# Performance work log

Measured on AMD Instinct MI355X. Metric: run time of the kernel, lower is better.

The kernel has to match this reference:

```python
import jax, jax.numpy as jnp
import numpy as np

N = 100000
E = 3200000
F_IN = 512
H = 128
C = 40


def gcn_conv(x, edge_index, edge_weight, W, b):
    """PyG GCNConv: x' = D^-1/2 (A+I) D^-1/2 (x W) + b, symmetric norm with self-loops."""
    n = x.shape[0]
    x = x @ W  # [N, H]
    row, col = edge_index[0], edge_index[1]
    sl = jnp.arange(n)
    row_f = jnp.concatenate([row, sl])
    col_f = jnp.concatenate([col, sl])
    w_f = jnp.concatenate([edge_weight, jnp.ones((n,), x.dtype)])
    deg = jax.ops.segment_sum(w_f, col_f, num_segments=n)  # in-degree incl. self-loop
    dinv = jnp.where(deg > 0, jax.lax.rsqrt(deg), 0.0)
    norm = dinv[row_f] * w_f * dinv[col_f]  # [E+N]
    msg = x[row_f] * norm[:, None]          # gather + scale
    out = jax.ops.segment_sum(msg, col_f, num_segments=n)  # scatter-add to targets
    return out + b


def setup_inputs() -> dict:
    key = jax.random.key(0)
    ks = jax.random.split(key, 12)
    inp = {
        "x": jax.random.normal(ks[0], (N, F_IN), jnp.float32),
        "edge_index": jax.random.randint(ks[1], (2, E), 0, N, jnp.int64),
        "edge_weight": jax.random.uniform(ks[2], (E,), jnp.float32),
        # first_lin
        "W1": jax.random.normal(ks[3], (F_IN, H), jnp.float32) / np.sqrt(F_IN),
        "b1": jnp.zeros((H,), jnp.float32),
        # conv layers (num_layers=2)
        "Wc1": jax.random.normal(ks[4], (H, H), jnp.float32) / np.sqrt(H),
        "bc1": jnp.zeros((H,), jnp.float32),
        "Wc2": jax.random.normal(ks[5], (H, H), jnp.float32) / np.sqrt(H),
        "bc2": jnp.zeros((H,), jnp.float32),
        # lin2
        "W2": jax.random.normal(ks[6], (H, C), jnp.float32) / np.sqrt(H),
        "b2": jnp.zeros((C,), jnp.float32),
        # wide layer
        "Ww": jax.random.normal(ks[7], (F_IN, C), jnp.float32) / np.sqrt(F_IN),
        "bw": jnp.zeros((C,), jnp.float32),
        # attention layer (-> 2 logits per node)
        "Wa": jax.random.normal(ks[8], (F_IN, 2), jnp.float32) / np.sqrt(F_IN),
        "ba": jnp.zeros((2,), jnp.float32),
    }
    return inp


def reference(x, edge_index, edge_weight, W1, b1, Wc1, bc1, Wc2, bc2, W2, b2, Ww, bw, Wa, ba):
    # deep branch (res_type=0.0, eval mode: dropout = identity)
    h = jax.nn.relu(x @ W1 + b1)
    h = jax.nn.relu(gcn_conv(h, edge_index, edge_weight, Wc1, bc1))
    h = jax.nn.relu(gcn_conv(h, edge_index, edge_weight, Wc2, bc2))
    deep_x = h @ W2 + b2  # [N, C]
    # wide branch on raw features
    wide_x = x @ Ww + bw  # [N, C]
    # attention fusion: softmax over 2 branch logits per node
    attn = jax.nn.softmax(x @ Wa + ba, axis=-1)  # [N, 2]
    out = deep_x * attn[:, 0:1] + wide_x * attn[:, 1:2]
    return out
```

## Files before the change

### kernel.cpp

```cpp
#include <hip/hip_runtime.h>
#include <hip/hip_bf16.h>
#include <cstdint>

#define N_NODES 100000
#define N_EDGES 3200000

typedef __attribute__((ext_vector_type(8))) short short8;
typedef __attribute__((ext_vector_type(4))) float floatx4;

#define FXS 8388608.0f
#define EA 320
#define EPB 10000
#define NBKT 391

__device__ __forceinline__ unsigned short f2bf(float f) {
    unsigned u = __float_as_uint(f);
    u += 0x7fff + ((u >> 16) & 1);
    return (unsigned short)(u >> 16);
}
__device__ __forceinline__ float bf2f(unsigned short s) {
    return __uint_as_float(((unsigned)s) << 16);
}
__device__ __forceinline__ float bflo(unsigned u) {
    return __uint_as_float(u << 16);
}
__device__ __forceinline__ float bfhi(unsigned u) {
    return __uint_as_float(u & 0xffff0000u);
}
__device__ __forceinline__ unsigned pack_bf2(float a, float b) {
    union { __hip_bfloat162 h2; unsigned u; } cv;
    cv.h2 = __float22bfloat162_rn(make_float2(a, b));
    return cv.u;
}

__global__ void setup_misc(const float* __restrict__ W1, const float* __restrict__ b1,
                           const float* __restrict__ Ww, const float* __restrict__ bw,
                           const float* __restrict__ Wa, const float* __restrict__ ba,
                           const float* __restrict__ Wc1, const float* __restrict__ Wc2,
                           const float* __restrict__ W2,
                           unsigned short* __restrict__ WcatT, float* __restrict__ bcat,
                           unsigned short* __restrict__ Wc1T, unsigned short* __restrict__ Wc2T,
                           unsigned short* __restrict__ W2T) {
    int bid = blockIdx.x, tid = threadIdx.x;
    if (bid < 192) {
        int c = bid;
        for (int kk = tid; kk < 512; kk += 256) {
            float v;
            if (c < 128)      v = W1[kk * 128 + c];
            else if (c < 168) v = Ww[kk * 40 + (c - 128)];
            else if (c < 170) v = Wa[kk * 2 + (c - 168)];
            else              v = 0.f;
            WcatT[(size_t)c * 512 + kk] = f2bf(v);
        }
        if (tid == 0) {
            float b;
            if (c < 128)      b = b1[c];
            else if (c < 168) b = bw[c - 128];
            else if (c < 170) b = ba[c - 168];
            else              b = 0.f;
            bcat[c] = b;
        }
    } else if (bid < 320) {
        int c = bid - 192;
        if (tid < 128) Wc1T[(size_t)c * 128 + tid] = f2bf(Wc1[tid * 128 + c]);
        else { int k = tid - 128; Wc2T[(size_t)c * 128 + k] = f2bf(Wc2[k * 128 + c]); }
    } else {
        int c = bid - 320;
        if (tid < 128)
            W2T[(size_t)c * 128 + tid] = (c < 40) ? f2bf(W2[tid * 40 + c])
                                                  : (unsigned short)0;
    }
}

template <int EPI, int NT, int AF32>
__device__ __forceinline__ void gemm_body(
    int mblk, const void* __restrict__ Avoid, const unsigned short* __restrict__ BT,
    int M, int K,
    unsigned short* __restrict__ C0, float* __restrict__ C1, float* __restrict__ C2,
    const float* __restrict__ bias, const float* __restrict__ rowscale) {
    constexpr int NB = 32 * NT;
    __shared__ __align__(16) unsigned short Ast[64 * 40];
    __shared__ __align__(16) unsigned short Bst[NB * 40];

    int tid = threadIdx.x;
    int m0 = mblk * 64;
    int wave = tid >> 6, lane = tid & 63;
    int quad = lane >> 4, mi = lane & 15;
    int wm = (wave >> 1) * 32;
    int wn = (wave & 1) * (16 * NT);

    int srow = tid >> 2;
    int sk8 = (tid & 3) * 8;

    int arow = m0 + srow; if (arow >= M) arow = M - 1;

    floatx4 acc[2][NT] = {};

    for (int kc = 0; kc < K; kc += 32) {
        if (AF32) {
            const float* Af = (const float*)Avoid;
            const float4* ap = (const float4*)(Af + (size_t)arow * K + kc + sk8);
            float4 f0 = ap[0], f1 = ap[1];
            uint4 pk;
            pk.x = pack_bf2(f0.x, f0.y);
            pk.y = pack_bf2(f0.z, f0.w);
            pk.z = pack_bf2(f1.x, f1.y);
            pk.w = pack_bf2(f1.z, f1.w);
            *(uint4*)&Ast[srow * 40 + sk8] = pk;
        } else {
            const unsigned short* Ab = (const unsigned short*)Avoid;
            uint4 av = *(const uint4*)(Ab + (size_t)arow * K + kc + sk8);
            *(uint4*)&Ast[srow * 40 + sk8] = av;
        }
#pragma unroll
        for (int i = tid; i < NB * 4; i += 256) {
            int brow = i >> 2;
            int bk8 = (i & 3) * 8;
            uint4 bv = *(const uint4*)(BT + (size_t)brow * K + kc + bk8);
            *(uint4*)&Bst[brow * 40 + bk8] = bv;
        }
        __syncthreads();

        short8 a0 = *(const short8*)&Ast[(wm + mi) * 40 + quad * 8];
        short8 a1 = *(const short8*)&Ast[(wm + 16 + mi) * 40 + quad * 8];
#pragma unroll
        for (int nt = 0; nt < NT; ++nt) {
            short8 b = *(const short8*)&Bst[(wn + nt * 16 + mi) * 40 + quad * 8];
            acc[0][nt] = __builtin_amdgcn_mfma_f32_16x16x32_bf16(a0, b, acc[0][nt], 0, 0, 0);
            acc[1][nt] = __builtin_amdgcn_mfma_f32_16x16x32_bf16(a1, b, acc[1][nt], 0, 0, 0);
        }
        __syncthreads();
    }

#pragma unroll
    for (int mt = 0; mt < 2; ++mt) {
#pragma unroll
        for (int nt = 0; nt < NT; ++nt) {
            floatx4 v = acc[mt][nt];
            int gn = wn + nt * 16 + mi;
#pragma unroll
            for (int r = 0; r < 4; ++r) {
                int gm = m0 + wm + mt * 16 + quad * 4 + r;
                if (gm >= M) continue;
                float val = v[r];
                if (EPI == 0) {
                    C0[(size_t)gm * 128 + gn] = f2bf(rowscale[gm] * val);
                } else if (EPI == 1) {
                    val += bias[gn];
                    if (gn < 128)      C0[(size_t)gm * 128 + gn] = f2bf(fmaxf(val, 0.f));
                    else if (gn < 168) C1[(size_t)gm * 40 + (gn - 128)] = val;
                    else if (gn < 170) C2[(size_t)gm * 2 + (gn - 168)] = val;
                } else {
                    if (gn < 40) {
                        float l0 = rowscale[gm * 2], l1 = rowscale[gm * 2 + 1];
                        float mx = fmaxf(l0, l1);
                        float e0 = __expf(l0 - mx), e1 = __expf(l1 - mx);
                        float inv = 1.f / (e0 + e1);
                        C1[(size_t)gm * 40 + gn] =
                            (val + bias[gn]) * (e0 * inv) +
                            C2[(size_t)gm * 40 + gn] * (e1 * inv);
                    }
                }
            }
        }
    }
}

__global__ __launch_bounds__(256) void megaA(
    const float* __restrict__ x, const unsigned short* __restrict__ WcatT,
    unsigned short* __restrict__ h0, float* __restrict__ wide, float* __restrict__ attnL,
    const float* __restrict__ bcat, const int* __restrict__ ei,
    int* __restrict__ histA, int M, int e) {
    int bid = blockIdx.x;
    if (bid >= EA) {
        gemm_body<1, 6, 1>(bid - EA, x, WcatT, M, 512, h0, wide, attnL, bcat, nullptr);
        return;
    }
    __shared__ unsigned lh[NBKT];
    int tid = threadIdx.x;
    for (int i = tid; i < NBKT; i += 256) lh[i] = 0;
    __syncthreads();
    int base = bid * EPB, end = base + EPB; if (end > e) end = e;
    for (int i = base + tid; i < end; i += 256) {
        int d = ei[e + i];
        atomicAdd(&lh[d >> 8], 1u);
    }
    __syncthreads();
    for (int k = tid; k < NBKT; k += 256) histA[k * EA + bid] = (int)lh[k];
}

__global__ __launch_bounds__(256) void scatterA(
    const int* __restrict__ ei, const float* __restrict__ ew,
    const int* __restrict__ offA, uint2* __restrict__ cs, int e) {
    int bid = blockIdx.x, tid = threadIdx.x;
    __shared__ unsigned lh[NBKT];
    __shared__ int lo[NBKT];
    for (int i = tid; i < NBKT; i += 256) { lh[i] = 0; lo[i] = offA[i * EA + bid]; }
    __syncthreads();
    int base = bid * EPB, end = base + EPB; if (end > e) end = e;
    for (int i = base + tid; i < end; i += 256) {
        int d = ei[e + i];
        int r = ei[i];
        float w = ew[i];
        int k = d >> 8;
        unsigned lr = atomicAdd(&lh[k], 1u);
        cs[lo[k] + (int)lr] = make_uint2((unsigned)r | ((unsigned)(d & 255) << 24),
                                         __float_as_uint(w));
    }
}

__global__ __launch_bounds__(1024) void passB1(
    const uint2* __restrict__ cs, const int* __restrict__ offA,
    int* __restrict__ cnt, unsigned* __restrict__ wsum, int n, int e) {
    int k = blockIdx.x, tid = threadIdx.x;
    __shared__ unsigned lc[256], lw[256];
    if (tid < 256) { lc[tid] = 0; lw[tid] = 0; }
    __syncthreads();
    int start = offA[k * EA];
    int end = (k == NBKT - 1) ? e : offA[(k + 1) * EA];
    for (int i = start + tid; i < end; i += 1024) {
        uint2 u = cs[i];
        int dlow = u.x >> 24;
        unsigned fx = (unsigned)(__uint_as_float(u.y) * FXS);
        atomicAdd(&lc[dlow], 1u);
        atomicAdd(&lw[dlow], fx);
    }
    __syncthreads();
    if (tid < 256) {
        int d = (k << 8) + tid;
        if (d < n) { cnt[d] = (int)lc[tid]; wsum[d] = lw[tid]; }
    }
}

__global__ void dinv_k(const unsigned* __restrict__ wsum, float* __restrict__ dinv, int n) {
    int i = blockIdx.x * 256 + threadIdx.x;
    if (i < n) dinv[i] = rsqrtf(1.0f + (float)wsum[i] * (1.0f / FXS));
}

__global__ __launch_bounds__(256) void megaB(
    const unsigned short* __restrict__ h0, const unsigned short* __restrict__ Wc1T,
    unsigned short* __restrict__ tmpB, const float* __restrict__ dinv,
    const uint2* __restrict__ cs, const int* __restrict__ offA,
    const int* __restrict__ ptr, uint2* __restrict__ edges, int M, int n, int e) {
    int bid = blockIdx.x;
    if (bid >= NBKT) {
        gemm_body<0, 4, 0>(bid - NBKT, h0, Wc1T, M, 128, tmpB, nullptr, nullptr, nullptr, dinv);
        return;
    }
    int k = bid, tid = threadIdx.x;
    __shared__ unsigned lc[256];
    __shared__ int lp[256];
    { lc[tid] = 0; int d = (k << 8) + tid; lp[tid] = (d < n) ? ptr[d] : 0; }
    __syncthreads();
    int start = offA[k * EA];
    int end = (k == NBKT - 1) ? e : offA[(k + 1) * EA];
    for (int i = start + tid; i < end; i += 256) {
        uint2 u = cs[i];
        int dlow = u.x >> 24;
        unsigned src = u.x & 0x00FFFFFFu;
        unsigned lr = atomicAdd(&lc[dlow], 1u);
        edges[lp[dlow] + (int)lr] = make_uint2(src, u.y);
    }
}

__global__ __launch_bounds__(256) void gemm_conv(
    const unsigned short* __restrict__ A, const unsigned short* __restrict__ BT,
    unsigned short* __restrict__ C0, const float* __restrict__ rowscale, int M) {
    gemm_body<0, 4, 0>(blockIdx.x, A, BT, M, 128, C0, nullptr, nullptr, nullptr, rowscale);
}

__global__ __launch_bounds__(256) void gemm_final(
    const unsigned short* __restrict__ A, const unsigned short* __restrict__ W2T,
    float* __restrict__ out, float* __restrict__ wide,
    const float* __restrict__ attnL, const float* __restrict__ b2, int M) {
    gemm_body<2, 2, 0>(blockIdx.x, A, W2T, M, 128, nullptr, out, wide, b2, attnL);
}

__global__ void scan1(const int* __restrict__ in, int* __restrict__ out,
                      int* __restrict__ bsum, int n) {
    __shared__ int s[1024];
    int tid = threadIdx.x;
    int i = blockIdx.x * 1024 + tid;
    int v = (i < n) ? in[i] : 0;
    s[tid] = v;
    __syncthreads();
    for (int off = 1; off < 1024; off <<= 1) {
        int t = (tid >= off) ? s[tid - off] : 0;
        __syncthreads();
        s[tid] += t;
        __syncthreads();
    }
    if (i < n) out[i] = s[tid] - v;
    if (tid == 1023) bsum[blockIdx.x] = s[1023];
}

__global__ void scan_bsums(int* bsum, int nb) {
    __shared__ int s[1024];
    int tid = threadIdx.x;
    int v = (tid < nb) ? bsum[tid] : 0;
    s[tid] = v;
    __syncthreads();
    for (int off = 1; off < 1024; off <<= 1) {
        int t = (tid >= off) ? s[tid - off] : 0;
        __syncthreads();
        s[tid] += t;
        __syncthreads();
    }
    if (tid < nb) bsum[tid] = s[tid] - v;
}

__global__ void scan_add(int* __restrict__ out, const int* __restrict__ bsum,
                         int n, int tailv) {
    int i = blockIdx.x * 1024 + threadIdx.x;
    if (i < n) out[i] += bsum[blockIdx.x];
    if (i == 0 && tailv >= 0) out[n] = tailv;
}

__global__ __launch_bounds__(256) void propagate(
    const unsigned int* __restrict__ tmp2,
    unsigned int* __restrict__ out2,
    const float* __restrict__ bias, const float* __restrict__ dinv,
    const int* __restrict__ ptr, const uint2* __restrict__ edges, int n) {
    int wave = threadIdx.x >> 6, lane = threadIdx.x & 63;
    int d = blockIdx.x * 4 + wave;
    if (d >= n) return;

    unsigned u = tmp2[(size_t)d * 64 + lane];
    float acc0 = bflo(u);
    float acc1 = bfhi(u);

    int p = ptr[d], p1 = ptr[d + 1];
    for (; p + 8 <= p1; p += 8) {
        uint2 q[8];
#pragma unroll
        for (int j = 0; j < 8; ++j) q[j] = edges[p + j];
        unsigned rv[8];
#pragma unroll
        for (int j = 0; j < 8; ++j) rv[j] = tmp2[(size_t)q[j].x * 64 + lane];
#pragma unroll
        for (int j = 0; j < 8; ++j) {
            float w = __uint_as_float(q[j].y);
            acc0 += w * bflo(rv[j]); acc1 += w * bfhi(rv[j]);
        }
    }
    for (; p < p1; ++p) {
        uint2 q = edges[p];
        unsigned a = tmp2[(size_t)q.x * 64 + lane];
        float w = __uint_as_float(q.y);
        acc0 += w * bflo(a); acc1 += w * bfhi(a);
    }
    float di = dinv[d];
    float v0 = fmaxf(di * acc0 + bias[2 * lane], 0.f);
    float v1 = fmaxf(di * acc1 + bias[2 * lane + 1], 0.f);
    out2[(size_t)d * 64 + lane] = (unsigned)f2bf(v0) | ((unsigned)f2bf(v1) << 16);
}

extern "C" void kernel_launch(void* const* d_in, const int* in_sizes, int n_in,
                              void* d_out, int out_size, void* d_ws, size_t ws_size,
                              hipStream_t stream) {
    (void)in_sizes; (void)n_in; (void)out_size; (void)ws_size;
    const float* x   = (const float*)d_in[0];
    const int*   ei  = (const int*)d_in[1];
    const float* ew  = (const float*)d_in[2];
    const float* W1  = (const float*)d_in[3];
    const float* b1  = (const float*)d_in[4];
    const float* Wc1 = (const float*)d_in[5];
    const float* bc1 = (const float*)d_in[6];
    const float* Wc2 = (const float*)d_in[7];
    const float* bc2 = (const float*)d_in[8];
    const float* W2  = (const float*)d_in[9];
    const float* b2  = (const float*)d_in[10];
    const float* Ww  = (const float*)d_in[11];
    const float* bw  = (const float*)d_in[12];
    const float* Wa  = (const float*)d_in[13];
    const float* ba  = (const float*)d_in[14];
    float* out = (float*)d_out;

    const int N = N_NODES, E = N_EDGES;
    char* ws = (char*)d_ws;
    size_t off = 0;
    auto alloc = [&](size_t bytes) -> void* {
        void* p = ws + off;
        off = (off + bytes + 255) & ~(size_t)255;
        return p;
    };
    unsigned short* bufA = (unsigned short*)alloc((size_t)N * 128 * 2);
    unsigned short* bufB = (unsigned short*)alloc((size_t)N * 128 * 2);
    float* wide  = (float*)alloc((size_t)N * 40 * 4);
    float* attnL = (float*)alloc((size_t)N * 2 * 4);
    float* dinv  = (float*)alloc((size_t)N * 4);
    int*   histA = (int*)alloc((size_t)NBKT * EA * 4);
    uint2* cs    = (uint2*)alloc((size_t)E * 8);
    int*   cnt   = (int*)alloc((size_t)N * 4);
    unsigned* wsum = (unsigned*)alloc((size_t)N * 4);
    int*   ptr   = (int*)alloc((size_t)(N + 1) * 4);
    int*   bsum  = (int*)alloc(1024 * 4);
    uint2* edges = (uint2*)alloc((size_t)E * 8);
    unsigned short* WcatT = (unsigned short*)alloc((size_t)192 * 512 * 2);
    unsigned short* Wc1T  = (unsigned short*)alloc((size_t)128 * 128 * 2);
    unsigned short* Wc2T  = (unsigned short*)alloc((size_t)128 * 128 * 2);
    unsigned short* W2T   = (unsigned short*)alloc((size_t)64 * 128 * 2);
    float* bcat  = (float*)alloc(192 * 4);

    const int MB = (N + 63) / 64;
    const int NHA = NBKT * EA;

    setup_misc<<<384, 256, 0, stream>>>(W1, b1, Ww, bw, Wa, ba, Wc1, Wc2, W2,
                                        WcatT, bcat, Wc1T, Wc2T, W2T);

    megaA<<<EA + MB, 256, 0, stream>>>(x, WcatT, bufA, wide, attnL, bcat,
                                       ei, histA, N, E);

    int nbA = (NHA + 1023) / 1024;
    scan1<<<nbA, 1024, 0, stream>>>(histA, histA, bsum, NHA);
    scan_bsums<<<1, 1024, 0, stream>>>(bsum, nbA);
    scan_add<<<nbA, 1024, 0, stream>>>(histA, bsum, NHA, -1);

    scatterA<<<EA, 256, 0, stream>>>(ei, ew, histA, cs, E);

    passB1<<<NBKT, 1024, 0, stream>>>(cs, histA, cnt, wsum, N, E);
    dinv_k<<<(N + 255) / 256, 256, 0, stream>>>(wsum, dinv, N);

    int nbC = (N + 1023) / 1024;
    scan1<<<nbC, 1024, 0, stream>>>(cnt, ptr, bsum, N);
    scan_bsums<<<1, 1024, 0, stream>>>(bsum, nbC);
    scan_add<<<nbC, 1024, 0, stream>>>(ptr, bsum, N, E);

    megaB<<<NBKT + MB, 256, 0, stream>>>(bufA, Wc1T, bufB, dinv,
                                         cs, histA, ptr, edges, N, N, E);
    propagate<<<(N + 3) / 4, 256, 0, stream>>>((const unsigned int*)bufB, (unsigned int*)bufA,
                                               bc1, dinv, ptr, edges, N);

    gemm_conv<<<MB, 256, 0, stream>>>(bufA, Wc2T, bufB, dinv, N);
    propagate<<<(N + 3) / 4, 256, 0, stream>>>((const unsigned int*)bufB, (unsigned int*)bufA,
                                               bc2, dinv, ptr, edges, N);

    gemm_final<<<MB, 256, 0, stream>>>(bufA, W2T, out, wide, attnL, b2, N);
}
```

Baseline: 752.7 us.

## Prefetch GEMM tiles into registers and fold CSR scan and dinv into passB1

The GEMM body now loads the next K-chunk of A and B into registers right after the barrier, so global loads overlap the MFMA work on the current chunk. passB1 now computes the per-node row pointers with an in-block prefix scan, starting from the bucket offset it already has, and writes dinv directly. This removes the dinv kernel and three scan launches along with the cnt and wsum buffers. The cost is extra register pressure in the GEMM and a serial shared-memory scan inside passB1.

```diff
diff --git a/kernel.cpp b/kernel.cpp
--- a/kernel.cpp
+++ b/kernel.cpp
@@ -79,6 +79,7 @@
     unsigned short* __restrict__ C0, float* __restrict__ C1, float* __restrict__ C2,
     const float* __restrict__ bias, const float* __restrict__ rowscale) {
     constexpr int NB = 32 * NT;
+    constexpr int RB = NT / 2;
     __shared__ __align__(16) unsigned short Ast[64 * 40];
     __shared__ __align__(16) unsigned short Bst[NB * 40];
 
@@ -94,32 +95,53 @@
 
     int arow = m0 + srow; if (arow >= M) arow = M - 1;
 
+    const float* Afp = (const float*)Avoid + (size_t)arow * K + sk8;
+    const unsigned short* Abp = (const unsigned short*)Avoid + (size_t)arow * K + sk8;
+    int brow[RB], bk8[RB];
+    const unsigned short* Bp[RB];
+#pragma unroll
+    for (int r = 0; r < RB; ++r) {
+        int i = tid + r * 256;
+        brow[r] = i >> 2;
+        bk8[r] = (i & 3) * 8;
+        Bp[r] = BT + (size_t)(i >> 2) * K + (i & 3) * 8;
+    }
+
+    float4 fA0, fA1; uint4 aR;
+    if (AF32) { fA0 = *(const float4*)(Afp); fA1 = *(const float4*)(Afp + 4); }
+    else      { aR = *(const uint4*)(Abp); }
+    uint4 bR[RB];
+#pragma unroll
+    for (int r = 0; r < RB; ++r) bR[r] = *(const uint4*)(Bp[r]);
+
     floatx4 acc[2][NT] = {};
 
     for (int kc = 0; kc < K; kc += 32) {
         if (AF32) {
-            const float* Af = (const float*)Avoid;
-            const float4* ap = (const float4*)(Af + (size_t)arow * K + kc + sk8);
-            float4 f0 = ap[0], f1 = ap[1];
             uint4 pk;
-            pk.x = pack_bf2(f0.x, f0.y);
-            pk.y = pack_bf2(f0.z, f0.w);
-            pk.z = pack_bf2(f1.x, f1.y);
-            pk.w = pack_bf2(f1.z, f1.w);
+            pk.x = pack_bf2(fA0.x, fA0.y);
+            pk.y = pack_bf2(fA0.z, fA0.w);
+            pk.z = pack_bf2(fA1.x, fA1.y);
+            pk.w = pack_bf2(fA1.z, fA1.w);
             *(uint4*)&Ast[srow * 40 + sk8] = pk;
         } else {
-            const unsigned short* Ab = (const unsigned short*)Avoid;
-            uint4 av = *(const uint4*)(Ab + (size_t)arow * K + kc + sk8);
-            *(uint4*)&Ast[srow * 40 + sk8] = av;
-        }
-#pragma unroll
-        for (int i = tid; i < NB * 4; i += 256) {
-            int brow = i >> 2;
-            int bk8 = (i & 3) * 8;
-            uint4 bv = *(const uint4*)(BT + (size_t)brow * K + kc + bk8);
-            *(uint4*)&Bst[brow * 40 + bk8] = bv;
-        }
-        __syncthreads();
+            *(uint4*)&Ast[srow * 40 + sk8] = aR;
+        }
+#pragma unroll
+        for (int r = 0; r < RB; ++r)
+            *(uint4*)&Bst[brow[r] * 40 + bk8[r]] = bR[r];
+        __syncthreads();
+
+        if (kc + 32 < K) {
+            if (AF32) {
+                fA0 = *(const float4*)(Afp + kc + 32);
+                fA1 = *(const float4*)(Afp + kc + 36);
+            } else {
+                aR = *(const uint4*)(Abp + kc + 32);
+            }
+#pragma unroll
+            for (int r = 0; r < RB; ++r) bR[r] = *(const uint4*)(Bp[r] + kc + 32);
+        }
 
         short8 a0 = *(const short8*)&Ast[(wm + mi) * 40 + quad * 8];
         short8 a1 = *(const short8*)&Ast[(wm + 16 + mi) * 40 + quad * 8];
@@ -211,9 +233,10 @@
 
 __global__ __launch_bounds__(1024) void passB1(
     const uint2* __restrict__ cs, const int* __restrict__ offA,
-    int* __restrict__ cnt, unsigned* __restrict__ wsum, int n, int e) {
+    int* __restrict__ ptr, float* __restrict__ dinv, int n, int e) {
     int k = blockIdx.x, tid = threadIdx.x;
     __shared__ unsigned lc[256], lw[256];
+    __shared__ int ls[256];
     if (tid < 256) { lc[tid] = 0; lw[tid] = 0; }
     __syncthreads();
     int start = offA[k * EA];
@@ -226,15 +249,23 @@
         atomicAdd(&lw[dlow], fx);
     }
     __syncthreads();
+    int v = (tid < 256) ? (int)lc[tid] : 0;
+    if (tid < 256) ls[tid] = v;
+    __syncthreads();
+    for (int off = 1; off < 256; off <<= 1) {
+        int t = (tid < 256 && tid >= off) ? ls[tid - off] : 0;
+        __syncthreads();
+        if (tid < 256) ls[tid] += t;
+        __syncthreads();
+    }
     if (tid < 256) {
         int d = (k << 8) + tid;
-        if (d < n) { cnt[d] = (int)lc[tid]; wsum[d] = lw[tid]; }
-    }
-}
-
-__global__ void dinv_k(const unsigned* __restrict__ wsum, float* __restrict__ dinv, int n) {
-    int i = blockIdx.x * 256 + threadIdx.x;
-    if (i < n) dinv[i] = rsqrtf(1.0f + (float)wsum[i] * (1.0f / FXS));
+        if (d < n) {
+            ptr[d]  = start + ls[tid] - v;
+            dinv[d] = rsqrtf(1.0f + (float)lw[tid] * (1.0f / FXS));
+        }
+    }
+    if (k == NBKT - 1 && tid == 0) ptr[n] = e;
 }
 
 __global__ __launch_bounds__(256) void megaB(
@@ -391,8 +422,6 @@
     float* dinv  = (float*)alloc((size_t)N * 4);
     int*   histA = (int*)alloc((size_t)NBKT * EA * 4);
     uint2* cs    = (uint2*)alloc((size_t)E * 8);
-    int*   cnt   = (int*)alloc((size_t)N * 4);
-    unsigned* wsum = (unsigned*)alloc((size_t)N * 4);
     int*   ptr   = (int*)alloc((size_t)(N + 1) * 4);
     int*   bsum  = (int*)alloc(1024 * 4);
     uint2* edges = (uint2*)alloc((size_t)E * 8);
@@ -418,13 +447,7 @@
 
     scatterA<<<EA, 256, 0, stream>>>(ei, ew, histA, cs, E);
 
-    passB1<<<NBKT, 1024, 0, stream>>>(cs, histA, cnt, wsum, N, E);
-    dinv_k<<<(N + 255) / 256, 256, 0, stream>>>(wsum, dinv, N);
-
-    int nbC = (N + 1023) / 1024;
-    scan1<<<nbC, 1024, 0, stream>>>(cnt, ptr, bsum, N);
-    scan_bsums<<<1, 1024, 0, stream>>>(bsum, nbC);
-    scan_add<<<nbC, 1024, 0, stream>>>(ptr, bsum, N, E);
+    passB1<<<NBKT, 1024, 0, stream>>>(cs, histA, ptr, dinv, N, E);
 
     megaB<<<NBKT + MB, 256, 0, stream>>>(bufA, Wc1T, bufB, dinv,
                                          cs, histA, ptr, edges, N, N, E);
```

After: 839.8 us. +11.6%, slower.

## Fuse CSR pointer scan and dinv into bucket pass, deepen propagate unroll

Applied to the files above, without the earlier changes.

The degree-count pass now computes an in-block exclusive prefix sum over its 256 destinations and offsets it by the bucket's global start, writing the CSR row pointers and dinv directly. This removes the separate dinv kernel and the three-kernel global scan over node counts. Separately, the propagate gather loop is unrolled to 16 edges with a 4-edge tail loop, so more neighbour-row loads are in flight per wave. The deeper unroll raises register pressure, and the in-block scan adds several barriers per block.

```diff
diff --git a/kernel.cpp b/kernel.cpp
--- a/kernel.cpp
+++ b/kernel.cpp
@@ -211,9 +211,10 @@
 
 __global__ __launch_bounds__(1024) void passB1(
     const uint2* __restrict__ cs, const int* __restrict__ offA,
-    int* __restrict__ cnt, unsigned* __restrict__ wsum, int n, int e) {
+    int* __restrict__ ptr, float* __restrict__ dinv, int n, int e) {
     int k = blockIdx.x, tid = threadIdx.x;
     __shared__ unsigned lc[256], lw[256];
+    __shared__ int ls[256];
     if (tid < 256) { lc[tid] = 0; lw[tid] = 0; }
     __syncthreads();
     int start = offA[k * EA];
@@ -226,15 +227,23 @@
         atomicAdd(&lw[dlow], fx);
     }
     __syncthreads();
+    int v = (tid < 256) ? (int)lc[tid] : 0;
+    if (tid < 256) ls[tid] = v;
+    __syncthreads();
+    for (int off = 1; off < 256; off <<= 1) {
+        int t = (tid < 256 && tid >= off) ? ls[tid - off] : 0;
+        __syncthreads();
+        if (tid < 256) ls[tid] += t;
+        __syncthreads();
+    }
     if (tid < 256) {
         int d = (k << 8) + tid;
-        if (d < n) { cnt[d] = (int)lc[tid]; wsum[d] = lw[tid]; }
-    }
-}
-
-__global__ void dinv_k(const unsigned* __restrict__ wsum, float* __restrict__ dinv, int n) {
-    int i = blockIdx.x * 256 + threadIdx.x;
-    if (i < n) dinv[i] = rsqrtf(1.0f + (float)wsum[i] * (1.0f / FXS));
+        if (d < n) {
+            ptr[d]  = start + ls[tid] - v;
+            dinv[d] = rsqrtf(1.0f + (float)lw[tid] * (1.0f / FXS));
+        }
+    }
+    if (k == NBKT - 1 && tid == 0) ptr[n] = e;
 }
 
 __global__ __launch_bounds__(256) void megaB(
@@ -330,15 +339,28 @@
     float acc1 = bfhi(u);
 
     int p = ptr[d], p1 = ptr[d + 1];
-    for (; p + 8 <= p1; p += 8) {
-        uint2 q[8];
-#pragma unroll
-        for (int j = 0; j < 8; ++j) q[j] = edges[p + j];
-        unsigned rv[8];
-#pragma unroll
-        for (int j = 0; j < 8; ++j) rv[j] = tmp2[(size_t)q[j].x * 64 + lane];
-#pragma unroll
-        for (int j = 0; j < 8; ++j) {
+    for (; p + 16 <= p1; p += 16) {
+        uint2 q[16];
+#pragma unroll
+        for (int j = 0; j < 16; ++j) q[j] = edges[p + j];
+        unsigned rv[16];
+#pragma unroll
+        for (int j = 0; j < 16; ++j) rv[j] = tmp2[(size_t)q[j].x * 64 + lane];
+#pragma unroll
+        for (int j = 0; j < 16; ++j) {
+            float w = __uint_as_float(q[j].y);
+            acc0 += w * bflo(rv[j]); acc1 += w * bfhi(rv[j]);
+        }
+    }
+    for (; p + 4 <= p1; p += 4) {
+        uint2 q[4];
+#pragma unroll
+        for (int j = 0; j < 4; ++j) q[j] = edges[p + j];
+        unsigned rv[4];
+#pragma unroll
+        for (int j = 0; j < 4; ++j) rv[j] = tmp2[(size_t)q[j].x * 64 + lane];
+#pragma unroll
+        for (int j = 0; j < 4; ++j) {
             float w = __uint_as_float(q[j].y);
             acc0 += w * bflo(rv[j]); acc1 += w * bfhi(rv[j]);
         }
@@ -391,8 +413,6 @@
     float* dinv  = (float*)alloc((size_t)N * 4);
     int*   histA = (int*)alloc((size_t)NBKT * EA * 4);
     uint2* cs    = (uint2*)alloc((size_t)E * 8);
-    int*   cnt   = (int*)alloc((size_t)N * 4);
-    unsigned* wsum = (unsigned*)alloc((size_t)N * 4);
     int*   ptr   = (int*)alloc((size_t)(N + 1) * 4);
     int*   bsum  = (int*)alloc(1024 * 4);
     uint2* edges = (uint2*)alloc((size_t)E * 8);
@@ -418,13 +438,7 @@
 
     scatterA<<<EA, 256, 0, stream>>>(ei, ew, histA, cs, E);
 
-    passB1<<<NBKT, 1024, 0, stream>>>(cs, histA, cnt, wsum, N, E);
-    dinv_k<<<(N + 255) / 256, 256, 0, stream>>>(wsum, dinv, N);
-
-    int nbC = (N + 1023) / 1024;
-    scan1<<<nbC, 1024, 0, stream>>>(cnt, ptr, bsum, N);
-    scan_bsums<<<1, 1024, 0, stream>>>(bsum, nbC);
-    scan_add<<<nbC, 1024, 0, stream>>>(ptr, bsum, N, E);
+    passB1<<<NBKT, 1024, 0, stream>>>(cs, histA, ptr, dinv, N, E);
 
     megaB<<<NBKT + MB, 256, 0, stream>>>(bufA, Wc1T, bufB, dinv,
                                          cs, histA, ptr, edges, N, N, E);
```

Measured after the change: 738.7 us. No clear change (-1.9%).
